# Kernel optimization log

Measured on AMD Instinct MI355X. Metric: run time of the kernel, lower is better.

Reference implementation:

```python
import jax, jax.numpy as jnp
import numpy as np

N, T, D, P, NB = 32768, 128, 32, 16, 15


def setup_inputs() -> dict:
    key = jax.random.key(0)
    ks = jax.random.split(key, 8)
    S = jax.random.normal(ks[0], (N, T, 1), dtype=jnp.float32)
    L_dyn = jax.random.normal(ks[1], (N, T, D), dtype=jnp.float32)
    C_static = jax.random.normal(ks[2], (N, P), dtype=jnp.float32)
    Y = jax.random.randint(ks[3], (N, T, 1), 0, 2).astype(jnp.float32)
    mask = jnp.ones((N, T), dtype=jnp.float32)
    return {
        "S": S, "L_dyn": L_dyn, "C_static": C_static, "Y": Y, "mask": mask,
        "psi": jnp.array([0.5], jnp.float32),
        "gamma_A": jnp.array([0.1], jnp.float32),
        "w_gamma_dyn": 0.05 * jax.random.normal(ks[4], (D,), dtype=jnp.float32),
        "w_gamma_static": 0.05 * jax.random.normal(ks[5], (P,), dtype=jnp.float32),
        "log_sigma_Z": jnp.array([-0.5], jnp.float32),
        "beta_0": jnp.array([-4.0], jnp.float32),
        "beta_Z": jnp.array([0.3], jnp.float32),
        "beta_bins": jnp.zeros((NB,), jnp.float32),
        "w_beta_dyn": 0.1 * jax.random.normal(ks[6], (D,), dtype=jnp.float32),
        "w_beta_static": 0.1 * jax.random.normal(ks[7], (P,), dtype=jnp.float32),
        "beta_time": jnp.array([0.03], jnp.float32),
    }


def reference(S, L_dyn, C_static, Y, mask, psi, gamma_A, w_gamma_dyn,
              w_gamma_static, log_sigma_Z, beta_0, beta_Z, beta_bins,
              w_beta_dyn, w_beta_static, beta_time):
    n, t_len = S.shape[0], S.shape[1]
    nb = beta_bins.shape[0]
    edges = jnp.linspace(-2.5, 2.5, nb + 1).astype(S.dtype)
    # torch.bucketize(s, edges[1:-1]) (right=False) == searchsorted side='left'
    idx = jnp.clip(jnp.searchsorted(edges[1:-1], S[..., 0], side='left'), 0, nb - 1)
    bin_eff = beta_bins[idx][..., None]            # (N,T,1) == (A_bin * beta_bins).sum(-1)
    sigma_sq = jnp.exp(log_sigma_Z)[0] ** 2        # sigma_Z^2
    gd = L_dyn @ w_gamma_dyn[:, None]              # (N,T,1) gamma_dyn(L)
    bd = L_dyn @ w_beta_dyn[:, None]               # (N,T,1) beta_dyn(L)
    gs = (C_static @ w_gamma_static)[:, None]      # (N,1) gamma_static(C)
    bs = (C_static @ w_beta_static)[:, None]       # (N,1) beta_static(C)
    tt = jnp.arange(t_len, dtype=S.dtype) / 30.0   # beta_time * (t/30)

    xs = (
        jnp.swapaxes(S, 0, 1),        # (T,N,1)
        jnp.swapaxes(gd, 0, 1),
        jnp.swapaxes(bd, 0, 1),
        jnp.swapaxes(bin_eff, 0, 1),
        jnp.swapaxes(Y, 0, 1),
        mask.T[:, :, None],           # (T,N,1)
        tt,
    )
    psi_s, gA, bZ, b0, bT = psi[0], gamma_A[0], beta_Z[0], beta_0[0], beta_time[0]

    def step(carry, x):
        Z_mean, Z_var, ll = carry
        A_t, gd_t, bd_t, be_t, Y_t, m_t, t_s = x
        # latent transition prior
        Z_pred_mean = psi_s * Z_mean + gA * A_t + gd_t + gs
        Z_pred_var = psi_s ** 2 * Z_var + sigma_sq
        # outcome probability
        logit = b0 + bZ * Z_pred_mean + be_t + bd_t + bs + bT * t_s
        prob = jax.nn.sigmoid(jnp.clip(logit, -20.0, 20.0))
        # approximate Kalman (Laplace) update from Y
        grad = (Y_t - prob) * bZ * m_t
        hess = bZ ** 2 * prob * (1.0 - prob) * m_t + 1e-6
        Z_post_var = 1.0 / (1.0 / (Z_pred_var + 1e-8) + hess)
        Z_post_mean = Z_pred_mean + Z_post_var * grad
        ll_t = ((Y_t * jnp.log(prob + 1e-10)
                 + (1.0 - Y_t) * jnp.log(1.0 - prob + 1e-10)) * m_t).sum()
        return (Z_post_mean, Z_post_var, ll + ll_t), (Z_post_mean, Z_post_var)

    init = (jnp.zeros((n, 1), S.dtype), jnp.ones((n, 1), S.dtype),
            jnp.zeros((), S.dtype))
    (_, _, ll), (Zf, Zv) = jax.lax.scan(step, init, xs)
    return jnp.swapaxes(Zf, 0, 1), jnp.swapaxes(Zv, 0, 1), ll
```

## Files before the change

### kernel.cpp

```cpp
#include <hip/hip_runtime.h>

#define T_LEN 128
#define NB_BINS 15
#define SEQS_PER_BLOCK 16

__global__ __launch_bounds__(256) void k_pre(
    const float4* __restrict__ L4,
    const float*  __restrict__ S,
    const float*  __restrict__ Y,
    const float*  __restrict__ M,
    const float4* __restrict__ C4,
    const float4* __restrict__ wgs4,
    const float4* __restrict__ wbs4,
    const float4* __restrict__ wgd4,
    const float4* __restrict__ wbd4,
    const float*  __restrict__ p_gA,
    const float*  __restrict__ p_b0,
    const float*  __restrict__ p_bbins,
    const float*  __restrict__ p_bT,
    float4* __restrict__ staged,
    int Nseq)
{
    __shared__ float4 tile[T_LEN][SEQS_PER_BLOCK + 1];
    __shared__ float sgs[SEQS_PER_BLOCK], sbs[SEQS_PER_BLOCK];
    __shared__ float sbins[NB_BINS];

    const int tid = threadIdx.x;
    if (tid < NB_BINS) sbins[tid] = p_bbins[tid];

    const int n0 = blockIdx.x * SEQS_PER_BLOCK;

    if (tid < SEQS_PER_BLOCK) {
        float gs = 0.0f, bs = 0.0f;
        #pragma unroll
        for (int i = 0; i < 4; ++i) {
            float4 c  = C4[(n0 + tid) * 4 + i];
            float4 wg = wgs4[i];
            float4 wb = wbs4[i];
            gs += c.x * wg.x + c.y * wg.y + c.z * wg.z + c.w * wg.w;
            bs += c.x * wb.x + c.y * wb.y + c.z * wb.z + c.w * wb.w;
        }
        sgs[tid] = gs; sbs[tid] = bs;
    }
    __syncthreads();

    const float gA   = p_gA[0];
    const float b0   = p_b0[0];
    const float bT30 = p_bT[0] * (1.0f / 30.0f);

    const int lane8 = tid & 7;
    const int gid   = tid >> 3;
    const float4 wg = wgd4[lane8];
    const float4 wb = wbd4[lane8];

    const size_t rowbase = (size_t)n0 * T_LEN;

    float4 v = L4[(rowbase + gid) * 8 + lane8];
    for (int it = 0; it < 64; ++it) {
        const int    lrow = it * 32 + gid;
        const size_t row  = rowbase + lrow;

        float4 vn = v;
        if (it + 1 < 64) vn = L4[(row + 32) * 8 + lane8];

        float g = v.x * wg.x + v.y * wg.y + v.z * wg.z + v.w * wg.w;
        float b = v.x * wb.x + v.y * wb.y + v.z * wb.z + v.w * wb.w;
        #pragma unroll
        for (int off = 1; off < 8; off <<= 1) {
            g += __shfl_xor(g, off, 64);
            b += __shfl_xor(b, off, 64);
        }

        const int nl = lrow >> 7;
        const int t  = lrow & 127;
        const float s_v = S[row];
        const float y_v = Y[row];
        const float m_v = M[row];
        int cnt = (int)fmaxf(0.0f, fminf(14.0f,
                      ceilf(fmaf(s_v, 3.0f, 7.5f)) - 1.0f));
        const float a = gA * s_v + g + sgs[nl];
        const float c = b0 + sbins[cnt] + b + sbs[nl] + bT30 * (float)t;

        if (lane8 == 0) tile[t][nl] = make_float4(a, c, y_v, m_v);
        v = vn;
    }
    __syncthreads();

    #pragma unroll
    for (int p = 0; p < 8; ++p) {
        const int idx = p * 256 + tid;
        const int t = idx >> 4, j = idx & 15;
        staged[(size_t)t * Nseq + n0 + j] = tile[t][j];
    }
}

__global__ __launch_bounds__(64) void k_scan(
    const float4* __restrict__ staged,
    const float*  __restrict__ p_psi,
    const float*  __restrict__ p_lsz,
    const float*  __restrict__ p_bZ,
    float4* __restrict__ Zf4,
    float4* __restrict__ Zv4,
    float*  __restrict__ ll_out,
    int Nseq)
{
    const int n = blockIdx.x * 64 + threadIdx.x;

    const float psi  = p_psi[0];
    const float e    = __expf(p_lsz[0]);
    const float sig2 = e * e;
    const float bZ   = p_bZ[0];
    const float psi2 = psi * psi;
    const float bZ2  = bZ * bZ;

    float zm = 0.0f, zvv = 1.0f, ll = 0.0f;

#define STEP(PK, PMOUT, PVOUT) do {                                       \
        const float zpm = fmaf(psi, zm, PK.x);                            \
        const float zpv = fmaf(psi2, zvv, sig2);                          \
        float logit = fmaf(bZ, zpm, PK.y);                                \
        logit = fminf(fmaxf(logit, -20.0f), 20.0f);                       \
        const float prob = __builtin_amdgcn_rcpf(1.0f + __expf(-logit));  \
        const float grad = (PK.z - prob) * bZ * PK.w;                     \
        const float hess = fmaf(bZ2 * prob * (1.0f - prob), PK.w, 1e-6f); \
        const float pvv  = __builtin_amdgcn_rcpf(                         \
                             __builtin_amdgcn_rcpf(zpv + 1e-8f) + hess);  \
        const float pmm  = fmaf(pvv, grad, zpm);                          \
        ll += (PK.z * __logf(prob + 1e-10f)                               \
             + (1.0f - PK.z) * __logf(1.0f - prob + 1e-10f)) * PK.w;      \
        zm = pmm; zvv = pvv; PMOUT = pmm; PVOUT = pvv;                    \
    } while (0)

#define LOADBUF(B0, B1, B2, B3, CIDX) do {                                \
        const int cc = (CIDX) > 31 ? 31 : (CIDX);                         \
        const float4* p = staged + (size_t)(cc * 4) * Nseq + n;           \
        B0 = p[0];                                                        \
        B1 = p[(size_t)Nseq];                                             \
        B2 = p[2 * (size_t)Nseq];                                         \
        B3 = p[3 * (size_t)Nseq];                                         \
    } while (0)

#define COMP(B0, B1, B2, B3, K) do {                                      \
        float pm0, pm1, pm2, pm3, pv0, pv1, pv2, pv3;                     \
        STEP(B0, pm0, pv0);                                               \
        STEP(B1, pm1, pv1);                                               \
        STEP(B2, pm2, pv2);                                               \
        STEP(B3, pm3, pv3);                                               \
        Zf4[(size_t)n * 32 + (K)] = make_float4(pm0, pm1, pm2, pm3);      \
        Zv4[(size_t)n * 32 + (K)] = make_float4(pv0, pv1, pv2, pv3);      \
    } while (0)

    float4 A0, A1, A2, A3, B0, B1, B2, B3, C0, C1, C2, C3;
    LOADBUF(A0, A1, A2, A3, 0);
    LOADBUF(B0, B1, B2, B3, 1);
    LOADBUF(C0, C1, C2, C3, 2);

    for (int k = 0; k < 30; k += 3) {
        COMP(A0, A1, A2, A3, k);     LOADBUF(A0, A1, A2, A3, k + 3);
        COMP(B0, B1, B2, B3, k + 1); LOADBUF(B0, B1, B2, B3, k + 4);
        COMP(C0, C1, C2, C3, k + 2); LOADBUF(C0, C1, C2, C3, k + 5);
    }
    COMP(A0, A1, A2, A3, 30);
    COMP(B0, B1, B2, B3, 31);
#undef COMP
#undef LOADBUF
#undef STEP

    #pragma unroll
    for (int off = 1; off < 64; off <<= 1) ll += __shfl_xor(ll, off, 64);
    if ((threadIdx.x & 63) == 0) atomicAdd(ll_out, ll);
}

extern "C" void kernel_launch(void* const* d_in, const int* in_sizes, int n_in,
                              void* d_out, int out_size, void* d_ws, size_t ws_size,
                              hipStream_t stream) {
    const float* S     = (const float*)d_in[0];
    const float* L     = (const float*)d_in[1];
    const float* C     = (const float*)d_in[2];
    const float* Y     = (const float*)d_in[3];
    const float* M     = (const float*)d_in[4];
    const float* psi   = (const float*)d_in[5];
    const float* gA    = (const float*)d_in[6];
    const float* wgd   = (const float*)d_in[7];
    const float* wgs   = (const float*)d_in[8];
    const float* lsz   = (const float*)d_in[9];
    const float* b0    = (const float*)d_in[10];
    const float* bZ    = (const float*)d_in[11];
    const float* bbins = (const float*)d_in[12];
    const float* wbd   = (const float*)d_in[13];
    const float* wbs   = (const float*)d_in[14];
    const float* bT    = (const float*)d_in[15];

    const int NT    = in_sizes[0];
    const int n_seq = NT / T_LEN;

    float* zf = (float*)d_out;
    float* zv = zf + NT;
    float* ll = zf + 2 * (size_t)NT;

    float4* staged = (float4*)d_ws;

    hipMemsetAsync((void*)ll, 0, sizeof(float), stream);

    k_pre<<<n_seq / SEQS_PER_BLOCK, 256, 0, stream>>>(
        reinterpret_cast<const float4*>(L),
        S, Y, M,
        reinterpret_cast<const float4*>(C),
        reinterpret_cast<const float4*>(wgs),
        reinterpret_cast<const float4*>(wbs),
        reinterpret_cast<const float4*>(wgd),
        reinterpret_cast<const float4*>(wbd),
        gA, b0, bbins, bT,
        staged, n_seq);

    k_scan<<<n_seq / 64, 64, 0, stream>>>(
        staged, psi, lsz, bZ,
        reinterpret_cast<float4*>(zf),
        reinterpret_cast<float4*>(zv),
        ll, n_seq);
}
```

Baseline: 194.7 us.

## Fuse precompute and scan kernels, keep staged tile in LDS

Merges the precompute and recurrence kernels into one. Each block keeps its per-timestep (a, c, y, m) tile in shared memory, and 16 threads per block run the 128-step scan directly from LDS. This removes the global staging buffer's write and read round trip and one kernel launch. The cost is that only 16 of 256 threads do the serial scan, which leaves one partially active wave per block during the latency-bound recurrence, and the output writes per thread become scattered. S, Y and M are now loaded only by lane 0 of each group of eight.

```diff
diff --git a/kernel.cpp b/kernel.cpp
--- a/kernel.cpp
+++ b/kernel.cpp
@@ -2,35 +2,38 @@
 
 #define T_LEN 128
 #define NB_BINS 15
-#define SEQS_PER_BLOCK 16
+#define SPB 16
 
-__global__ __launch_bounds__(256) void k_pre(
-    const float4* __restrict__ L4,
+__global__ __launch_bounds__(256) void k_all(
     const float*  __restrict__ S,
     const float*  __restrict__ Y,
     const float*  __restrict__ M,
+    const float4* __restrict__ L4,
     const float4* __restrict__ C4,
     const float4* __restrict__ wgs4,
     const float4* __restrict__ wbs4,
     const float4* __restrict__ wgd4,
     const float4* __restrict__ wbd4,
+    const float*  __restrict__ p_psi,
     const float*  __restrict__ p_gA,
+    const float*  __restrict__ p_lsz,
     const float*  __restrict__ p_b0,
+    const float*  __restrict__ p_bZ,
     const float*  __restrict__ p_bbins,
     const float*  __restrict__ p_bT,
-    float4* __restrict__ staged,
-    int Nseq)
+    float4* __restrict__ Zf4,
+    float4* __restrict__ Zv4,
+    float*  __restrict__ ll_out)
 {
-    __shared__ float4 tile[T_LEN][SEQS_PER_BLOCK + 1];
-    __shared__ float sgs[SEQS_PER_BLOCK], sbs[SEQS_PER_BLOCK];
+    __shared__ float4 tile[T_LEN][SPB + 1];
+    __shared__ float sgs[SPB], sbs[SPB];
     __shared__ float sbins[NB_BINS];
 
     const int tid = threadIdx.x;
+    const int n0  = blockIdx.x * SPB;
+
     if (tid < NB_BINS) sbins[tid] = p_bbins[tid];
-
-    const int n0 = blockIdx.x * SEQS_PER_BLOCK;
-
-    if (tid < SEQS_PER_BLOCK) {
+    if (tid < SPB) {
         float gs = 0.0f, bs = 0.0f;
         #pragma unroll
         for (int i = 0; i < 4; ++i) {
@@ -52,7 +55,6 @@
     const int gid   = tid >> 3;
     const float4 wg = wgd4[lane8];
     const float4 wb = wbd4[lane8];
-
     const size_t rowbase = (size_t)n0 * T_LEN;
 
     float4 v = L4[(rowbase + gid) * 8 + lane8];
@@ -63,6 +65,9 @@
         float4 vn = v;
         if (it + 1 < 64) vn = L4[(row + 32) * 8 + lane8];
 
+        float s_v = 0.0f, y_v = 0.0f, m_v = 0.0f;
+        if (lane8 == 0) { s_v = S[row]; y_v = Y[row]; m_v = M[row]; }
+
         float g = v.x * wg.x + v.y * wg.y + v.z * wg.z + v.w * wg.w;
         float b = v.x * wb.x + v.y * wb.y + v.z * wb.z + v.w * wb.w;
         #pragma unroll
@@ -71,104 +76,61 @@
             b += __shfl_xor(b, off, 64);
         }
 
-        const int nl = lrow >> 7;
-        const int t  = lrow & 127;
-        const float s_v = S[row];
-        const float y_v = Y[row];
-        const float m_v = M[row];
-        int cnt = (int)fmaxf(0.0f, fminf(14.0f,
-                      ceilf(fmaf(s_v, 3.0f, 7.5f)) - 1.0f));
-        const float a = gA * s_v + g + sgs[nl];
-        const float c = b0 + sbins[cnt] + b + sbs[nl] + bT30 * (float)t;
-
-        if (lane8 == 0) tile[t][nl] = make_float4(a, c, y_v, m_v);
+        if (lane8 == 0) {
+            const int nl = lrow >> 7;
+            const int t  = lrow & 127;
+            int cnt = (int)fmaxf(0.0f, fminf(14.0f,
+                          ceilf(fmaf(s_v, 3.0f, 7.5f)) - 1.0f));
+            const float a = gA * s_v + g + sgs[nl];
+            const float c = b0 + sbins[cnt] + b + sbs[nl] + bT30 * (float)t;
+            tile[t][nl] = make_float4(a, c, y_v, m_v);
+        }
         v = vn;
     }
     __syncthreads();
 
-    #pragma unroll
-    for (int p = 0; p < 8; ++p) {
-        const int idx = p * 256 + tid;
-        const int t = idx >> 4, j = idx & 15;
-        staged[(size_t)t * Nseq + n0 + j] = tile[t][j];
+    float ll = 0.0f;
+    if (tid < SPB) {
+        const float psi  = p_psi[0];
+        const float e    = __expf(p_lsz[0]);
+        const float sig2 = e * e;
+        const float bZ   = p_bZ[0];
+        const float psi2 = psi * psi;
+        const float bZ2  = bZ * bZ;
+
+        float zm = 0.0f, zvv = 1.0f;
+        const int    nl = tid;
+        const size_t ob = (size_t)(n0 + nl) * 32;
+
+        for (int cnk = 0; cnk < 16; ++cnk) {
+            float pm[8], pv[8];
+            #pragma unroll
+            for (int j = 0; j < 8; ++j) {
+                const float4 pk = tile[cnk * 8 + j][nl];
+                const float zpm = fmaf(psi, zm, pk.x);
+                const float zpv = fmaf(psi2, zvv, sig2);
+                float logit = fmaf(bZ, zpm, pk.y);
+                logit = fminf(fmaxf(logit, -20.0f), 20.0f);
+                const float prob = __builtin_amdgcn_rcpf(1.0f + __expf(-logit));
+                const float grad = (pk.z - prob) * bZ * pk.w;
+                const float hess = fmaf(bZ2 * prob * (1.0f - prob), pk.w, 1e-6f);
+                const float pvv  = __builtin_amdgcn_rcpf(
+                                     __builtin_amdgcn_rcpf(zpv + 1e-8f) + hess);
+                const float pmm  = fmaf(pvv, grad, zpm);
+                ll += (pk.z * __logf(prob + 1e-10f)
+                     + (1.0f - pk.z) * __logf(1.0f - prob + 1e-10f)) * pk.w;
+                zm = pmm; zvv = pvv; pm[j] = pmm; pv[j] = pvv;
+            }
+            Zf4[ob + cnk * 2]     = make_float4(pm[0], pm[1], pm[2], pm[3]);
+            Zf4[ob + cnk * 2 + 1] = make_float4(pm[4], pm[5], pm[6], pm[7]);
+            Zv4[ob + cnk * 2]     = make_float4(pv[0], pv[1], pv[2], pv[3]);
+            Zv4[ob + cnk * 2 + 1] = make_float4(pv[4], pv[5], pv[6], pv[7]);
+        }
     }
-}
-
-__global__ __launch_bounds__(64) void k_scan(
-    const float4* __restrict__ staged,
-    const float*  __restrict__ p_psi,
-    const float*  __restrict__ p_lsz,
-    const float*  __restrict__ p_bZ,
-    float4* __restrict__ Zf4,
-    float4* __restrict__ Zv4,
-    float*  __restrict__ ll_out,
-    int Nseq)
-{
-    const int n = blockIdx.x * 64 + threadIdx.x;
-
-    const float psi  = p_psi[0];
-    const float e    = __expf(p_lsz[0]);
-    const float sig2 = e * e;
-    const float bZ   = p_bZ[0];
-    const float psi2 = psi * psi;
-    const float bZ2  = bZ * bZ;
-
-    float zm = 0.0f, zvv = 1.0f, ll = 0.0f;
-
-#define STEP(PK, PMOUT, PVOUT) do {                                       \
-        const float zpm = fmaf(psi, zm, PK.x);                            \
-        const float zpv = fmaf(psi2, zvv, sig2);                          \
-        float logit = fmaf(bZ, zpm, PK.y);                                \
-        logit = fminf(fmaxf(logit, -20.0f), 20.0f);                       \
-        const float prob = __builtin_amdgcn_rcpf(1.0f + __expf(-logit));  \
-        const float grad = (PK.z - prob) * bZ * PK.w;                     \
-        const float hess = fmaf(bZ2 * prob * (1.0f - prob), PK.w, 1e-6f); \
-        const float pvv  = __builtin_amdgcn_rcpf(                         \
-                             __builtin_amdgcn_rcpf(zpv + 1e-8f) + hess);  \
-        const float pmm  = fmaf(pvv, grad, zpm);                          \
-        ll += (PK.z * __logf(prob + 1e-10f)                               \
-             + (1.0f - PK.z) * __logf(1.0f - prob + 1e-10f)) * PK.w;      \
-        zm = pmm; zvv = pvv; PMOUT = pmm; PVOUT = pvv;                    \
-    } while (0)
-
-#define LOADBUF(B0, B1, B2, B3, CIDX) do {                                \
-        const int cc = (CIDX) > 31 ? 31 : (CIDX);                         \
-        const float4* p = staged + (size_t)(cc * 4) * Nseq + n;           \
-        B0 = p[0];                                                        \
-        B1 = p[(size_t)Nseq];                                             \
-        B2 = p[2 * (size_t)Nseq];                                         \
-        B3 = p[3 * (size_t)Nseq];                                         \
-    } while (0)
-
-#define COMP(B0, B1, B2, B3, K) do {                                      \
-        float pm0, pm1, pm2, pm3, pv0, pv1, pv2, pv3;                     \
-        STEP(B0, pm0, pv0);                                               \
-        STEP(B1, pm1, pv1);                                               \
-        STEP(B2, pm2, pv2);                                               \
-        STEP(B3, pm3, pv3);                                               \
-        Zf4[(size_t)n * 32 + (K)] = make_float4(pm0, pm1, pm2, pm3);      \
-        Zv4[(size_t)n * 32 + (K)] = make_float4(pv0, pv1, pv2, pv3);      \
-    } while (0)
-
-    float4 A0, A1, A2, A3, B0, B1, B2, B3, C0, C1, C2, C3;
-    LOADBUF(A0, A1, A2, A3, 0);
-    LOADBUF(B0, B1, B2, B3, 1);
-    LOADBUF(C0, C1, C2, C3, 2);
-
-    for (int k = 0; k < 30; k += 3) {
-        COMP(A0, A1, A2, A3, k);     LOADBUF(A0, A1, A2, A3, k + 3);
-        COMP(B0, B1, B2, B3, k + 1); LOADBUF(B0, B1, B2, B3, k + 4);
-        COMP(C0, C1, C2, C3, k + 2); LOADBUF(C0, C1, C2, C3, k + 5);
-    }
-    COMP(A0, A1, A2, A3, 30);
-    COMP(B0, B1, B2, B3, 31);
-#undef COMP
-#undef LOADBUF
-#undef STEP
 
     #pragma unroll
     for (int off = 1; off < 64; off <<= 1) ll += __shfl_xor(ll, off, 64);
-    if ((threadIdx.x & 63) == 0) atomicAdd(ll_out, ll);
+    if (tid == 0) atomicAdd(ll_out, ll);
 }
 
 extern "C" void kernel_launch(void* const* d_in, const int* in_sizes, int n_in,
@@ -198,24 +160,18 @@
     float* zv = zf + NT;
     float* ll = zf + 2 * (size_t)NT;
 
-    float4* staged = (float4*)d_ws;
-
     hipMemsetAsync((void*)ll, 0, sizeof(float), stream);
 
-    k_pre<<<n_seq / SEQS_PER_BLOCK, 256, 0, stream>>>(
+    k_all<<<n_seq / SPB, 256, 0, stream>>>(
+        S, Y, M,
         reinterpret_cast<const float4*>(L),
-        S, Y, M,
         reinterpret_cast<const float4*>(C),
         reinterpret_cast<const float4*>(wgs),
         reinterpret_cast<const float4*>(wbs),
         reinterpret_cast<const float4*>(wgd),
         reinterpret_cast<const float4*>(wbd),
-        gA, b0, bbins, bT,
-        staged, n_seq);
-
-    k_scan<<<n_seq / 64, 64, 0, stream>>>(
-        staged, psi, lsz, bZ,
+        psi, gA, lsz, b0, bZ, bbins, bT,
         reinterpret_cast<float4*>(zf),
         reinterpret_cast<float4*>(zv),
-        ll, n_seq);
+        ll);
 }
```

Result: no change. 193.7 us (-0.5%).

## Split static projection, grid-stride preprocessing, and 4-way redundant scan per sequence

Applied to the files above, without the earlier changes.

Moves the static covariate projections into a separate kernel. The preprocessing kernel becomes a grid-stride loop that writes staged float4 values directly, without the shared-memory transpose tile. The scan kernel now gives each sequence 4 threads that all run the full recurrence redundantly, and each thread keeps and stores only one quarter of the timestep outputs. This spreads the strided loads and stores over more waves and widens the output writes, at the cost of four times the transcendental and recurrence work. The direct staged writes are scattered 16-byte stores rather than coalesced tile flushes.

```diff
diff --git a/kernel.cpp b/kernel.cpp
--- a/kernel.cpp
+++ b/kernel.cpp
@@ -2,16 +2,35 @@
 
 #define T_LEN 128
 #define NB_BINS 15
-#define SEQS_PER_BLOCK 16
+
+__global__ __launch_bounds__(256) void k_static(
+    const float4* __restrict__ C4,
+    const float4* __restrict__ wgs4,
+    const float4* __restrict__ wbs4,
+    float* __restrict__ gs_out, float* __restrict__ bs_out, int n_seq)
+{
+    int n = blockIdx.x * blockDim.x + threadIdx.x;
+    if (n >= n_seq) return;
+    float gs = 0.0f, bs = 0.0f;
+    #pragma unroll
+    for (int i = 0; i < 4; ++i) {
+        float4 c  = C4[n * 4 + i];
+        float4 wg = wgs4[i];
+        float4 wb = wbs4[i];
+        gs += c.x * wg.x + c.y * wg.y + c.z * wg.z + c.w * wg.w;
+        bs += c.x * wb.x + c.y * wb.y + c.z * wb.z + c.w * wb.w;
+    }
+    gs_out[n] = gs;
+    bs_out[n] = bs;
+}
 
 __global__ __launch_bounds__(256) void k_pre(
     const float4* __restrict__ L4,
     const float*  __restrict__ S,
     const float*  __restrict__ Y,
     const float*  __restrict__ M,
-    const float4* __restrict__ C4,
-    const float4* __restrict__ wgs4,
-    const float4* __restrict__ wbs4,
+    const float*  __restrict__ gs_in,
+    const float*  __restrict__ bs_in,
     const float4* __restrict__ wgd4,
     const float4* __restrict__ wbd4,
     const float*  __restrict__ p_gA,
@@ -19,49 +38,37 @@
     const float*  __restrict__ p_bbins,
     const float*  __restrict__ p_bT,
     float4* __restrict__ staged,
-    int Nseq)
+    int total_rows, int Nseq)
 {
-    __shared__ float4 tile[T_LEN][SEQS_PER_BLOCK + 1];
-    __shared__ float sgs[SEQS_PER_BLOCK], sbs[SEQS_PER_BLOCK];
     __shared__ float sbins[NB_BINS];
-
-    const int tid = threadIdx.x;
-    if (tid < NB_BINS) sbins[tid] = p_bbins[tid];
-
-    const int n0 = blockIdx.x * SEQS_PER_BLOCK;
-
-    if (tid < SEQS_PER_BLOCK) {
-        float gs = 0.0f, bs = 0.0f;
-        #pragma unroll
-        for (int i = 0; i < 4; ++i) {
-            float4 c  = C4[(n0 + tid) * 4 + i];
-            float4 wg = wgs4[i];
-            float4 wb = wbs4[i];
-            gs += c.x * wg.x + c.y * wg.y + c.z * wg.z + c.w * wg.w;
-            bs += c.x * wb.x + c.y * wb.y + c.z * wb.z + c.w * wb.w;
-        }
-        sgs[tid] = gs; sbs[tid] = bs;
-    }
+    if (threadIdx.x < NB_BINS) sbins[threadIdx.x] = p_bbins[threadIdx.x];
     __syncthreads();
 
     const float gA   = p_gA[0];
     const float b0   = p_b0[0];
     const float bT30 = p_bT[0] * (1.0f / 30.0f);
 
+    const int tid   = blockIdx.x * blockDim.x + threadIdx.x;
     const int lane8 = tid & 7;
-    const int gid   = tid >> 3;
     const float4 wg = wgd4[lane8];
     const float4 wb = wbd4[lane8];
 
-    const size_t rowbase = (size_t)n0 * T_LEN;
-
-    float4 v = L4[(rowbase + gid) * 8 + lane8];
-    for (int it = 0; it < 64; ++it) {
-        const int    lrow = it * 32 + gid;
-        const size_t row  = rowbase + lrow;
-
+    const int group   = tid >> 3;
+    const int ngroups = (gridDim.x * blockDim.x) >> 3;
+
+    int row = group;
+    float4 v = L4[(size_t)row * 8 + lane8];
+    float s_v = 0.0f, y_v = 0.0f, m_v = 0.0f;
+    if (lane8 == 0) { s_v = S[row]; y_v = Y[row]; m_v = M[row]; }
+
+    for (; row < total_rows; row += ngroups) {
+        const int nrow = row + ngroups;
         float4 vn = v;
-        if (it + 1 < 64) vn = L4[(row + 32) * 8 + lane8];
+        float sn = s_v, yn = y_v, mn = m_v;
+        if (nrow < total_rows) {
+            vn = L4[(size_t)nrow * 8 + lane8];
+            if (lane8 == 0) { sn = S[nrow]; yn = Y[nrow]; mn = M[nrow]; }
+        }
 
         float g = v.x * wg.x + v.y * wg.y + v.z * wg.z + v.w * wg.w;
         float b = v.x * wb.x + v.y * wb.y + v.z * wb.z + v.w * wb.w;
@@ -71,30 +78,20 @@
             b += __shfl_xor(b, off, 64);
         }
 
-        const int nl = lrow >> 7;
-        const int t  = lrow & 127;
-        const float s_v = S[row];
-        const float y_v = Y[row];
-        const float m_v = M[row];
-        int cnt = (int)fmaxf(0.0f, fminf(14.0f,
-                      ceilf(fmaf(s_v, 3.0f, 7.5f)) - 1.0f));
-        const float a = gA * s_v + g + sgs[nl];
-        const float c = b0 + sbins[cnt] + b + sbs[nl] + bT30 * (float)t;
-
-        if (lane8 == 0) tile[t][nl] = make_float4(a, c, y_v, m_v);
-        v = vn;
+        if (lane8 == 0) {
+            const int n = row >> 7;
+            const int t = row & 127;
+            int cnt = (int)fmaxf(0.0f, fminf(14.0f,
+                          ceilf(fmaf(s_v, 3.0f, 7.5f)) - 1.0f));
+            const float a = gA * s_v + g + gs_in[n];
+            const float c = b0 + sbins[cnt] + b + bs_in[n] + bT30 * (float)t;
+            staged[(size_t)t * Nseq + n] = make_float4(a, c, y_v, m_v);
+        }
+        v = vn; s_v = sn; y_v = yn; m_v = mn;
     }
-    __syncthreads();
-
-    #pragma unroll
-    for (int p = 0; p < 8; ++p) {
-        const int idx = p * 256 + tid;
-        const int t = idx >> 4, j = idx & 15;
-        staged[(size_t)t * Nseq + n0 + j] = tile[t][j];
-    }
-}
-
-__global__ __launch_bounds__(64) void k_scan(
+}
+
+__global__ __launch_bounds__(256) void k_scan(
     const float4* __restrict__ staged,
     const float*  __restrict__ p_psi,
     const float*  __restrict__ p_lsz,
@@ -104,7 +101,10 @@
     float*  __restrict__ ll_out,
     int Nseq)
 {
-    const int n = blockIdx.x * 64 + threadIdx.x;
+    const int tid = threadIdx.x;
+    const int g   = tid >> 2;
+    const int s   = tid & 3;
+    const int n   = blockIdx.x * 64 + g;
 
     const float psi  = p_psi[0];
     const float e    = __expf(p_lsz[0]);
@@ -114,8 +114,18 @@
     const float bZ2  = bZ * bZ;
 
     float zm = 0.0f, zvv = 1.0f, ll = 0.0f;
-
-#define STEP(PK, PMOUT, PVOUT) do {                                       \
+    float m0 = 0.f, m1 = 0.f, m2 = 0.f, m3 = 0.f;
+    float v0 = 0.f, v1 = 0.f, v2 = 0.f, v3 = 0.f;
+
+    const size_t NS = (size_t)Nseq;
+
+#define LOADH(A,B,C,D,E,F,G,H, tb) do {                                   \
+        const float4* p = staged + (size_t)(tb) * NS + n;                 \
+        A = p[0];      B = p[NS];     C = p[2*NS];  D = p[3*NS];          \
+        E = p[4*NS];   F = p[5*NS];   G = p[6*NS];  H = p[7*NS];          \
+    } while (0)
+
+#define CSTEP(PK, CH, SM, SV) do {                                        \
         const float zpm = fmaf(psi, zm, PK.x);                            \
         const float zpv = fmaf(psi2, zvv, sig2);                          \
         float logit = fmaf(bZ, zpm, PK.y);                                \
@@ -126,49 +136,46 @@
         const float pvv  = __builtin_amdgcn_rcpf(                         \
                              __builtin_amdgcn_rcpf(zpv + 1e-8f) + hess);  \
         const float pmm  = fmaf(pvv, grad, zpm);                          \
-        ll += (PK.z * __logf(prob + 1e-10f)                               \
-             + (1.0f - PK.z) * __logf(1.0f - prob + 1e-10f)) * PK.w;      \
-        zm = pmm; zvv = pvv; PMOUT = pmm; PVOUT = pvv;                    \
+        if (s == (CH)) {                                                  \
+            SM = pmm; SV = pvv;                                           \
+            ll += (PK.z * __logf(prob + 1e-10f)                           \
+                 + (1.0f - PK.z) * __logf(1.0f - prob + 1e-10f)) * PK.w;  \
+        }                                                                 \
+        zm = pmm; zvv = pvv;                                              \
     } while (0)
 
-#define LOADBUF(B0, B1, B2, B3, CIDX) do {                                \
-        const int cc = (CIDX) > 31 ? 31 : (CIDX);                         \
-        const float4* p = staged + (size_t)(cc * 4) * Nseq + n;           \
-        B0 = p[0];                                                        \
-        B1 = p[(size_t)Nseq];                                             \
-        B2 = p[2 * (size_t)Nseq];                                         \
-        B3 = p[3 * (size_t)Nseq];                                         \
+#define COMPH(A,B,C,D,E,F,G,H, c0, c1) do {                               \
+        CSTEP(A, c0, m0, v0); CSTEP(B, c0, m1, v1);                       \
+        CSTEP(C, c0, m2, v2); CSTEP(D, c0, m3, v3);                       \
+        CSTEP(E, c1, m0, v0); CSTEP(F, c1, m1, v1);                       \
+        CSTEP(G, c1, m2, v2); CSTEP(H, c1, m3, v3);                       \
     } while (0)
 
-#define COMP(B0, B1, B2, B3, K) do {                                      \
-        float pm0, pm1, pm2, pm3, pv0, pv1, pv2, pv3;                     \
-        STEP(B0, pm0, pv0);                                               \
-        STEP(B1, pm1, pv1);                                               \
-        STEP(B2, pm2, pv2);                                               \
-        STEP(B3, pm3, pv3);                                               \
-        Zf4[(size_t)n * 32 + (K)] = make_float4(pm0, pm1, pm2, pm3);      \
-        Zv4[(size_t)n * 32 + (K)] = make_float4(pv0, pv1, pv2, pv3);      \
-    } while (0)
-
-    float4 A0, A1, A2, A3, B0, B1, B2, B3, C0, C1, C2, C3;
-    LOADBUF(A0, A1, A2, A3, 0);
-    LOADBUF(B0, B1, B2, B3, 1);
-    LOADBUF(C0, C1, C2, C3, 2);
-
-    for (int k = 0; k < 30; k += 3) {
-        COMP(A0, A1, A2, A3, k);     LOADBUF(A0, A1, A2, A3, k + 3);
-        COMP(B0, B1, B2, B3, k + 1); LOADBUF(B0, B1, B2, B3, k + 4);
-        COMP(C0, C1, C2, C3, k + 2); LOADBUF(C0, C1, C2, C3, k + 5);
+    float4 P0, P1, P2, P3, P4, P5, P6, P7;
+    float4 Q0, Q1, Q2, Q3, Q4, Q5, Q6, Q7;
+
+    LOADH(P0,P1,P2,P3,P4,P5,P6,P7, 0);
+
+    for (int Q = 0; Q < 8; ++Q) {
+        const int tb1 = 16 * Q + 8;
+        LOADH(Q0,Q1,Q2,Q3,Q4,Q5,Q6,Q7, tb1);
+        COMPH(P0,P1,P2,P3,P4,P5,P6,P7, 0, 1);
+
+        const int tb0 = (Q < 7) ? (16 * Q + 16) : 112;
+        LOADH(P0,P1,P2,P3,P4,P5,P6,P7, tb0);
+        COMPH(Q0,Q1,Q2,Q3,Q4,Q5,Q6,Q7, 2, 3);
+
+        const size_t ob = (size_t)n * 32 + Q * 4 + s;
+        Zf4[ob] = make_float4(m0, m1, m2, m3);
+        Zv4[ob] = make_float4(v0, v1, v2, v3);
     }
-    COMP(A0, A1, A2, A3, 30);
-    COMP(B0, B1, B2, B3, 31);
-#undef COMP
-#undef LOADBUF
-#undef STEP
+#undef COMPH
+#undef CSTEP
+#undef LOADH
 
     #pragma unroll
     for (int off = 1; off < 64; off <<= 1) ll += __shfl_xor(ll, off, 64);
-    if ((threadIdx.x & 63) == 0) atomicAdd(ll_out, ll);
+    if ((tid & 63) == 0) atomicAdd(ll_out, ll);
 }
 
 extern "C" void kernel_launch(void* const* d_in, const int* in_sizes, int n_in,
@@ -199,21 +206,26 @@
     float* ll = zf + 2 * (size_t)NT;
 
     float4* staged = (float4*)d_ws;
+    float*  gs_ws  = (float*)(staged + NT);
+    float*  bs_ws  = gs_ws + n_seq;
 
     hipMemsetAsync((void*)ll, 0, sizeof(float), stream);
 
-    k_pre<<<n_seq / SEQS_PER_BLOCK, 256, 0, stream>>>(
-        reinterpret_cast<const float4*>(L),
-        S, Y, M,
+    k_static<<<(n_seq + 255) / 256, 256, 0, stream>>>(
         reinterpret_cast<const float4*>(C),
         reinterpret_cast<const float4*>(wgs),
         reinterpret_cast<const float4*>(wbs),
+        gs_ws, bs_ws, n_seq);
+
+    k_pre<<<2048, 256, 0, stream>>>(
+        reinterpret_cast<const float4*>(L),
+        S, Y, M, gs_ws, bs_ws,
         reinterpret_cast<const float4*>(wgd),
         reinterpret_cast<const float4*>(wbd),
         gA, b0, bbins, bT,
-        staged, n_seq);
-
-    k_scan<<<n_seq / 64, 64, 0, stream>>>(
+        staged, NT, n_seq);
+
+    k_scan<<<n_seq / 64, 256, 0, stream>>>(
         staged, psi, lsz, bZ,
         reinterpret_cast<float4*>(zf),
         reinterpret_cast<float4*>(zv),
```

After: 234.6 us. 1.2x slower.
